# Kernel tuning notes

Hardware: AMD Instinct MI355X
Metric: run time of the kernel (lower is better)

Reference implementation:

```python
import jax, jax.numpy as jnp
import numpy as np

B, L, D, NHEADS, P = 64, 256, 768, 8, 3
VOCAB, DEP, NLAYERS = 30522, 45, 2
LAM = 0.5


def _forward(src_mask, aspect_mask, lex, attention_mask,
             tok_emb, seg_emb, pool_w, pool_b, ln_a, ln_b,
             dep_emb, fc1_w, fc1_b, fc2_w, fc2_b,
             aq_w, aq_b, ak_w, ak_b, lq_w, lq_b, lk_w, lk_b, root_w,
             gcn_w, gcn_b, fc3_w, fc3_b, cls_w, cls_b, vlin_w,
             text_bert_indices, bert_segments_ids, ori_tag, head):
    b, l = text_bert_indices.shape
    d = tok_emb.shape[1]
    dk = d // NHEADS
    NEG = jnp.float32(-1e30)
    # stand-in BERT encoder: token + segment embeddings, tanh pooler on [CLS]
    seq = tok_emb[text_bert_indices] + seg_emb[bert_segments_ids]
    pooled = jnp.tanh(seq[:, 0] @ pool_w + pool_b)
    # torch LayerNorm variant: unbiased std (ddof=1)
    mean = seq.mean(-1, keepdims=True)
    std = jnp.std(seq, axis=-1, keepdims=True, ddof=1)
    gcn_in = ln_a * (seq - mean) / (std + 1e-6) + ln_b
    # in-place fmask[:,0]=1 mutates src_mask storage in torch -> effective mask
    sm = src_mask.at[:, 0].set(1.0)
    # dependency-tag score -> per-token softmax -> scatter into [L,L] adjacency
    dep_h = jax.nn.relu(dep_emb[ori_tag] @ fc1_w + fc1_b)
    dep_s = (dep_h @ fc2_w + fc2_b)[..., 0]                      # [B,L]
    dep_feat = jax.nn.softmax(dep_s * sm + (1.0 - sm) * NEG, axis=1)
    to_idx = jnp.arange(1, l)
    fro = head[:, :l - 1]                                        # [B,L-1]
    b_idx = jnp.arange(b)[:, None]
    vals = dep_feat[:, :l - 1]
    dep_adj = jnp.ones((b, l, l), jnp.float32)
    dep_adj = dep_adj.at[b_idx, fro, to_idx[None, :]].set(vals)
    dep_adj = dep_adj.at[b_idx, to_idx[None, :], fro].set(vals)
    # multi-head attention-as-adjacency (returns softmax weights only)
    q = (gcn_in @ aq_w + aq_b).reshape(b, l, NHEADS, dk).transpose(0, 2, 1, 3)
    k = (gcn_in @ ak_w + ak_b).reshape(b, l, NHEADS, dk).transpose(0, 2, 1, 3)
    scores = jnp.einsum('bhqd,bhkd->bhqk', q, k) / (jnp.sqrt(jnp.float32(dk)) + 1e-9)
    scores = jnp.where(sm[:, None, None, :] == 0, jnp.float32(-1e9), scores)
    adj_ag = jax.nn.softmax(scores, axis=-1).mean(axis=1)        # [B,L,L]
    eye = jnp.eye(l, dtype=jnp.float32)
    adj_ag = (adj_ag * (1.0 - eye) + eye) * sm[:, :, None]
    # structured latent attention (stand-in for missing StructuredAtt):
    # masked bilinear attention biased by dep_adj + root attention loss
    q2 = gcn_in @ lq_w + lq_b
    k2 = gcn_in @ lk_w + lk_b
    lat = jnp.einsum('bqd,bkd->bqk', q2, k2) / jnp.sqrt(jnp.float32(d))
    lat = lat + dep_adj + (1.0 - sm)[:, None, :] * (-10000.0)
    adj_latent = jax.nn.softmax(lat, axis=-1)
    root_p = jax.nn.softmax((gcn_in @ root_w)[..., 0] * sm + (1.0 - sm) * NEG, axis=1)
    loss_root = -jnp.mean(jnp.log(jnp.sum(root_p * aspect_mask, axis=1) + 1e-9))
    adj_latent = (adj_latent * (1.0 - eye) + eye) * sm[:, :, None]
    # gated dual-adjacency GCN layers
    H_l = gcn_in
    I_sem = gcn_in
    for layer in range(gcn_w.shape[0]):
        g_l = jax.nn.sigmoid(H_l)
        I_sem = (adj_ag @ H_l) @ gcn_w[layer] + gcn_b[layer]
        I_lat = (adj_latent @ H_l) @ gcn_w[layer] + gcn_b[layer]
        g = jax.nn.sigmoid(I_lat)
        lam_g = LAM * g
        I_com = (1.0 - lam_g) * I_sem + lam_g * I_lat
        H_out = jax.nn.relu(I_com @ fc3_w + fc3_b)
        H_l = g_l * H_out + (1.0 - g_l) * H_l
    # readout
    asp_wn = aspect_mask.sum(axis=1, keepdims=True)              # [B,1]
    m3 = sm[:, :, None]
    h_l = H_l * m3
    h_sem = I_sem * m3
    beta = jnp.einsum('bqd,bkd->bqk', h_l, h_sem) / 1000.0
    attn_o = jax.nn.softmax(beta.sum(axis=1, keepdims=True), axis=2)  # [B,1,L]
    outputs = (attn_o @ I_sem)[:, 0]                             # [B,D]
    sem_pool = (I_sem * aspect_mask[:, :, None]).sum(axis=1) / (asp_wn + 1e-9)
    final = jnp.concatenate([outputs, sem_pool, pooled], axis=-1)  # [B,3D]
    logits = final @ cls_w + cls_b
    e = (H_l @ vlin_w)[..., 0]
    lw = jax.nn.softmax(e, axis=1) * 50.0
    lw = lw * sm.at[:, 0].set(0.0)
    lexicon_loss = jnp.mean((lw - lex) ** 2)
    return logits, loss_root, lexicon_loss


def setup_inputs() -> dict:
    key = jax.random.key(0)
    ks = jax.random.split(key, 24)
    s = 0.02
    n = lambda i, shape: jax.random.normal(ks[i], shape, dtype=jnp.float32) * s
    inp = {}
    inp['text_bert_indices'] = jax.random.randint(ks[0], (B, L), 0, VOCAB, dtype=jnp.int32)
    inp['bert_segments_ids'] = jnp.zeros((B, L), jnp.int32)
    inp['attention_mask'] = jnp.ones((B, L), jnp.float32)
    inp['src_mask'] = jnp.ones((B, L), jnp.float32)
    inp['aspect_mask'] = jax.random.randint(ks[1], (B, L), 0, 2).astype(jnp.float32)
    inp['lex'] = jax.random.uniform(ks[2], (B, L), dtype=jnp.float32)
    inp['ori_tag'] = jax.random.randint(ks[3], (B, L), 0, DEP, dtype=jnp.int32)
    inp['head'] = jax.random.randint(ks[4], (B, L), 0, L, dtype=jnp.int32)
    inp['tok_emb'] = n(5, (VOCAB, D)); inp['seg_emb'] = n(6, (2, D))
    inp['pool_w'] = n(7, (D, D)); inp['pool_b'] = jnp.zeros((D,), jnp.float32)
    inp['ln_a'] = jnp.ones((D,), jnp.float32); inp['ln_b'] = jnp.zeros((D,), jnp.float32)
    inp['dep_emb'] = n(8, (DEP, 300))
    inp['fc1_w'] = n(9, (300, 256)); inp['fc1_b'] = jnp.zeros((256,), jnp.float32)
    inp['fc2_w'] = n(10, (256, 1)); inp['fc2_b'] = jnp.zeros((1,), jnp.float32)
    inp['aq_w'] = n(11, (D, D)); inp['aq_b'] = jnp.zeros((D,), jnp.float32)
    inp['ak_w'] = n(12, (D, D)); inp['ak_b'] = jnp.zeros((D,), jnp.float32)
    inp['lq_w'] = n(13, (D, D)); inp['lq_b'] = jnp.zeros((D,), jnp.float32)
    inp['lk_w'] = n(14, (D, D)); inp['lk_b'] = jnp.zeros((D,), jnp.float32)
    inp['root_w'] = n(15, (D, 1))
    inp['gcn_w'] = n(16, (NLAYERS, D, D)); inp['gcn_b'] = jnp.zeros((NLAYERS, D), jnp.float32)
    inp['fc3_w'] = n(17, (D, D)); inp['fc3_b'] = jnp.zeros((D,), jnp.float32)
    inp['cls_w'] = n(18, (3 * D, P)); inp['cls_b'] = jnp.zeros((P,), jnp.float32)
    inp['vlin_w'] = n(19, (D, 1))
    return inp


def reference(text_bert_indices, bert_segments_ids, attention_mask, src_mask, aspect_mask, lex,
              ori_tag, head, tok_emb, seg_emb, pool_w, pool_b, ln_a, ln_b, dep_emb,
              fc1_w, fc1_b, fc2_w, fc2_b, aq_w, aq_b, ak_w, ak_b, lq_w, lq_b, lk_w, lk_b,
              root_w, gcn_w, gcn_b, fc3_w, fc3_b, cls_w, cls_b, vlin_w):
    return _forward(src_mask, aspect_mask, lex, attention_mask,
                    tok_emb, seg_emb, pool_w, pool_b, ln_a, ln_b,
                    dep_emb, fc1_w, fc1_b, fc2_w, fc2_b,
                    aq_w, aq_b, ak_w, ak_b, lq_w, lq_b, lk_w, lk_b, root_w,
                    gcn_w, gcn_b, fc3_w, fc3_b, cls_w, cls_b, vlin_w,
                    text_bert_indices, bert_segments_ids, ori_tag, head)
```

## Files before the change

### kernel.cpp

```cpp
#include <hip/hip_runtime.h>
#include <hip/hip_bf16.h>
#include <math.h>

#define DI __device__ __forceinline__

constexpr int cB = 64, cL = 256, cD = 768;
constexpr long BLD = (long)cB * cL * cD;
constexpr long BLL = (long)cB * cL * cL;
constexpr long cLL = (long)cL * cL;
constexpr long cLD = (long)cL * cD;

typedef __attribute__((ext_vector_type(8))) short b8;
typedef __attribute__((ext_vector_type(4))) float f4;

#define GLDS(g, l)                                                    \
  __builtin_amdgcn_global_load_lds(                                   \
      (const __attribute__((address_space(1))) void*)(g),             \
      (__attribute__((address_space(3))) void*)(l), 16, 0, 0)

#define SCB __builtin_amdgcn_sched_barrier(0)
DI void rbar() { SCB; __builtin_amdgcn_s_barrier(); SCB; }
DI void lbar() {
  asm volatile("s_waitcnt lgkmcnt(0)" ::: "memory");
  SCB;
  __builtin_amdgcn_s_barrier();
  SCB;
}

DI float wsum(float v) {
#pragma unroll
  for (int o = 32; o > 0; o >>= 1) v += __shfl_down(v, o, 64);
  return v;
}
DI float wsum_all(float v) {
#pragma unroll
  for (int m = 32; m > 0; m >>= 1) v += __shfl_xor(v, m, 64);
  return v;
}
DI float wmaxr(float v) {
#pragma unroll
  for (int o = 32; o > 0; o >>= 1) v = fmaxf(v, __shfl_down(v, o, 64));
  return v;
}
DI float blockSum(float v) {
  __shared__ float sh[4];
  v = wsum(v);
  __syncthreads();
  if ((threadIdx.x & 63) == 0) sh[threadIdx.x >> 6] = v;
  __syncthreads();
  return sh[0] + sh[1] + sh[2] + sh[3];
}
DI float blockMax(float v) {
  __shared__ float sh[4];
  v = wmaxr(v);
  __syncthreads();
  if ((threadIdx.x & 63) == 0) sh[threadIdx.x >> 6] = v;
  __syncthreads();
  return fmaxf(fmaxf(sh[0], sh[1]), fmaxf(sh[2], sh[3]));
}
DI float sigf(float x) { return 1.f / (1.f + expf(-x)); }

template <int OBF, int RELU, int BIAS, int EPI, int SWZ>
__global__ __launch_bounds__(256, 2) void bgemm(
    const __hip_bfloat16* __restrict__ A, const __hip_bfloat16* __restrict__ BT,
    void* __restrict__ Cv, const float* __restrict__ bias,
    float* __restrict__ auxf, __hip_bfloat16* __restrict__ auxb,
    int K, int lda, int ldb, int ldc,
    int zshift, int zmask, long sA1, long sA2, long sB1, long sB2, long sC,
    int czdiv) {
  __shared__ __hip_bfloat16 Asp[128 * 32];
  __shared__ __hip_bfloat16 Bsp[128 * 32];
  int bx = blockIdx.x, by = blockIdx.y;
  if (SWZ) {
    int gx = gridDim.x;
    int nb = gx * gridDim.y;
    int id = by * gx + bx;
    int cpx = nb >> 3;
    id = (id & 7) * cpx + (id >> 3);
    bx = id % gx;
    by = id / gx;
  }
  int z = blockIdx.z;
  A += (long)(z >> zshift) * sA1 + (long)(z & zmask) * sA2;
  BT += (long)(z >> zshift) * sB1 + (long)(z & zmask) * sB2;
  int tid = threadIdx.x;
  int lane = tid & 63, w = tid >> 6;
  int wr = w >> 1, wc = w & 1;
  int l16 = lane & 15, q = lane >> 4;
  int m0 = by << 7, n0 = bx << 7;

  int fm = tid >> 2, fq = tid & 3;
  const __hip_bfloat16* Ap0 = A + (long)(m0 + fm) * lda + fq * 8;
  const __hip_bfloat16* Ap1 = A + (long)(m0 + fm + 64) * lda + fq * 8;
  const __hip_bfloat16* Bp0 = BT + (long)(n0 + fm) * ldb + fq * 8;
  const __hip_bfloat16* Bp1 = BT + (long)(n0 + fm + 64) * ldb + fq * 8;
  char* Aw0 = (char*)Asp + (w << 10);
  char* Aw1 = (char*)Asp + 4096 + (w << 10);
  char* Bw0 = (char*)Bsp + (w << 10);
  char* Bw1 = (char*)Bsp + 4096 + (w << 10);

  f4 acc[4][4];
#pragma unroll
  for (int i = 0; i < 4; i++)
#pragma unroll
    for (int j = 0; j < 4; j++) acc[i][j] = (f4){0.f, 0.f, 0.f, 0.f};

  for (int k0 = 0; k0 < K; k0 += 32) {
    GLDS(Ap0 + k0, Aw0);
    GLDS(Ap1 + k0, Aw1);
    GLDS(Bp0 + k0, Bw0);
    GLDS(Bp1 + k0, Bw1);
    __syncthreads();
    b8 af[4], bf[4];
#pragma unroll
    for (int i = 0; i < 4; i++)
      af[i] = *(const b8*)&Asp[(wr * 64 + i * 16 + l16) * 32 + q * 8];
#pragma unroll
    for (int j = 0; j < 4; j++)
      bf[j] = *(const b8*)&Bsp[(wc * 64 + j * 16 + l16) * 32 + q * 8];
#pragma unroll
    for (int i = 0; i < 4; i++)
#pragma unroll
      for (int j = 0; j < 4; j++)
        acc[i][j] = __builtin_amdgcn_mfma_f32_16x16x32_bf16(af[i], bf[j], acc[i][j], 0, 0, 0);
    __syncthreads();
  }
  if (EPI == 4) {
#pragma unroll
    for (int j = 0; j < 4; j++) {
      int n = n0 + wc * 64 + j * 16 + l16;
#pragma unroll
      for (int i = 0; i < 4; i++) {
        int m = m0 + wr * 64 + i * 16 + (q << 2);
        __hip_bfloat16 t4[4];
#pragma unroll
        for (int r = 0; r < 4; r++) t4[r] = __float2bfloat16(acc[i][j][r]);
        long bidx = (long)(m >> 8) * sC + (long)n * cL + (m & 255);
        *(uint2*)&((__hip_bfloat16*)Cv)[bidx] = *(uint2*)t4;
      }
    }
    return;
  }
  long cz = (long)(z >> czdiv) * sC;
#pragma unroll
  for (int j = 0; j < 4; j++) {
    int n = n0 + wc * 64 + j * 16 + l16;
    float bv = BIAS ? bias[n] : 0.f;
#pragma unroll
    for (int i = 0; i < 4; i++) {
#pragma unroll
      for (int r = 0; r < 4; r++) {
        int m = m0 + wr * 64 + i * 16 + q * 4 + r;
        long idx = cz + (long)m * ldc + n;
        float v = acc[i][j][r] + bv;
        if (EPI == 0) {
          if (RELU) v = fmaxf(v, 0.f);
          if (OBF)
            ((__hip_bfloat16*)Cv)[idx] = __float2bfloat16(v);
          else
            ((float*)Cv)[idx] = v;
        } else {
          v = fmaxf(v, 0.f);
          float h = __bfloat162float(auxb[idx]);
          float g = sigf(h);
          float o = h + g * (v - h);
          auxb[idx] = __float2bfloat16(o);
          if (auxf) auxf[idx] = o;
        }
      }
    }
  }
}

__global__ __launch_bounds__(256, 2) void bgemm_dual(
    const __hip_bfloat16* __restrict__ A1g, const __hip_bfloat16* __restrict__ A2g,
    const __hip_bfloat16* __restrict__ BTg, float* __restrict__ IsemF,
    __hip_bfloat16* __restrict__ Icb, const float* __restrict__ bias,
    int write_isem) {
  __shared__ __hip_bfloat16 A1sp[128 * 32];
  __shared__ __hip_bfloat16 A2sp[128 * 32];
  __shared__ __hip_bfloat16 Bsp[128 * 32];
  int id = (blockIdx.z * 2 + blockIdx.y) * 6 + blockIdx.x;
  id = (id & 7) * 96 + (id >> 3);
  int bx = id % 6, t = id / 6;
  int by = t & 1, z = t >> 1;
  const __hip_bfloat16* A1 = A1g + (long)z * cLL;
  const __hip_bfloat16* A2 = A2g + (long)z * cLL;
  const __hip_bfloat16* BT = BTg + (long)z * cLD;
  int tid = threadIdx.x;
  int lane = tid & 63, w = tid >> 6;
  int wr = w >> 1, wc = w & 1;
  int l16 = lane & 15, q = lane >> 4;
  int m0 = by << 7, n0 = bx << 7;

  int fm = tid >> 2, fq = tid & 3;
  const __hip_bfloat16* A1p0 = A1 + (long)(m0 + fm) * cL + fq * 8;
  const __hip_bfloat16* A1p1 = A1p0 + 64L * cL;
  const __hip_bfloat16* A2p0 = A2 + (long)(m0 + fm) * cL + fq * 8;
  const __hip_bfloat16* A2p1 = A2p0 + 64L * cL;
  const __hip_bfloat16* Bp0 = BT + (long)(n0 + fm) * cL + fq * 8;
  const __hip_bfloat16* Bp1 = Bp0 + 64L * cL;
  char* w10 = (char*)A1sp + (w << 10);
  char* w11 = (char*)A1sp + 4096 + (w << 10);
  char* w20 = (char*)A2sp + (w << 10);
  char* w21 = (char*)A2sp + 4096 + (w << 10);
  char* wb0 = (char*)Bsp + (w << 10);
  char* wb1 = (char*)Bsp + 4096 + (w << 10);

  f4 ac1[4][4], ac2[4][4];
#pragma unroll
  for (int i = 0; i < 4; i++)
#pragma unroll
    for (int j = 0; j < 4; j++) {
      ac1[i][j] = (f4){0.f, 0.f, 0.f, 0.f};
      ac2[i][j] = (f4){0.f, 0.f, 0.f, 0.f};
    }

  for (int k0 = 0; k0 < cL; k0 += 32) {
    GLDS(A1p0 + k0, w10);
    GLDS(A1p1 + k0, w11);
    GLDS(A2p0 + k0, w20);
    GLDS(A2p1 + k0, w21);
    GLDS(Bp0 + k0, wb0);
    GLDS(Bp1 + k0, wb1);
    __syncthreads();
    b8 a1f[4], a2f[4], bf[4];
#pragma unroll
    for (int i = 0; i < 4; i++) {
      a1f[i] = *(const b8*)&A1sp[(wr * 64 + i * 16 + l16) * 32 + q * 8];
      a2f[i] = *(const b8*)&A2sp[(wr * 64 + i * 16 + l16) * 32 + q * 8];
    }
#pragma unroll
    for (int j = 0; j < 4; j++)
      bf[j] = *(const b8*)&Bsp[(wc * 64 + j * 16 + l16) * 32 + q * 8];
#pragma unroll
    for (int i = 0; i < 4; i++)
#pragma unroll
      for (int j = 0; j < 4; j++) {
        ac1[i][j] = __builtin_amdgcn_mfma_f32_16x16x32_bf16(a1f[i], bf[j], ac1[i][j], 0, 0, 0);
        ac2[i][j] = __builtin_amdgcn_mfma_f32_16x16x32_bf16(a2f[i], bf[j], ac2[i][j], 0, 0, 0);
      }
    __syncthreads();
  }
  long cz = (long)z * cLD;
#pragma unroll
  for (int j = 0; j < 4; j++) {
    int n = n0 + wc * 64 + j * 16 + l16;
    float bv = bias[n];
#pragma unroll
    for (int i = 0; i < 4; i++) {
#pragma unroll
      for (int r = 0; r < 4; r++) {
        int m = m0 + wr * 64 + i * 16 + q * 4 + r;
        long idx = cz + (long)m * cD + n;
        float is = ac1[i][j][r] + bv;
        float il = ac2[i][j][r] + bv;
        float g = 0.5f * sigf(il);
        Icb[idx] = __float2bfloat16(is + g * (il - is));
        if (write_isem) IsemF[idx] = is;
      }
    }
  }
}

__global__ __launch_bounds__(256, 2) void k_qkadj2(
    const __hip_bfloat16* __restrict__ qkb, const float* __restrict__ src_mask,
    const int* __restrict__ headv, const float* __restrict__ df,
    __hip_bfloat16* __restrict__ outAag, __hip_bfloat16* __restrict__ outAlat) {
  __shared__ __hip_bfloat16 Qs[2][64 * 32];
  __shared__ __hip_bfloat16 Ks[2][256 * 32];
  __shared__ float red[4][64];
  int id = (blockIdx.z * gridDim.y + blockIdx.y) * gridDim.x + blockIdx.x;
  int W = (id & 7) * 64 + (id >> 3);
  const bool lat = W >= 256;
  int rem = W & 255;
  const int b = rem >> 2, m0 = (rem & 3) << 6;
  const int QOFF = lat ? 1536 : 0;
  const int KOFF = lat ? 2304 : 768;
  const float scale = lat ? (1.f / sqrtf(768.f)) : (1.f / (sqrtf(96.f) + 1e-9f));
  const int tid = threadIdx.x, lane = tid & 63, w = tid >> 6;
  const int l16 = lane & 15, q = lane >> 4;
  const long rowbase = (long)b * cL;
  const __hip_bfloat16* Qg =
      qkb + (rowbase + m0 + (tid >> 2)) * 3072 + (tid & 3) * 8 + QOFF;
  const __hip_bfloat16* Kg =
      qkb + (rowbase + (tid >> 2)) * 3072 + (tid & 3) * 8 + KOFF;

  float smj[4];
#pragma unroll
  for (int j = 0; j < 4; j++) {
    int col = w * 64 + j * 16 + l16;
    smj[j] = (col == 0) ? 1.f : src_mask[b * cL + col];
  }

  f4 sa[4][4], aag[4][4];
#pragma unroll
  for (int i = 0; i < 4; i++)
#pragma unroll
    for (int j = 0; j < 4; j++) {
      sa[i][j] = (f4){0.f, 0.f, 0.f, 0.f};
      aag[i][j] = (f4){0.f, 0.f, 0.f, 0.f};
    }

  auto STAGE = [&](int s, int p) {
    GLDS(Qg + s * 32, (char*)Qs[p] + (w << 10));
#pragma unroll
    for (int u = 0; u < 4; u++)
      GLDS(Kg + (long)u * 196608 + s * 32, (char*)Ks[p] + u * 4096 + (w << 10));
  };

  STAGE(0, 0);
  STAGE(1, 1);

  for (int s = 0; s < 24; s++) {
    const int p = s & 1;
    if (s < 23) {
      asm volatile("s_waitcnt vmcnt(5)" ::: "memory");
    } else {
      asm volatile("s_waitcnt vmcnt(0)" ::: "memory");
    }
    rbar();
    if (!lat && (s % 3) == 0) {
#pragma unroll
      for (int i = 0; i < 4; i++)
#pragma unroll
        for (int j = 0; j < 4; j++) sa[i][j] = (f4){0.f, 0.f, 0.f, 0.f};
    }
    b8 af[4], bf[4];
#pragma unroll
    for (int i = 0; i < 4; i++)
      af[i] = *(const b8*)&Qs[p][(i * 16 + l16) * 32 + q * 8];
#pragma unroll
    for (int j = 0; j < 4; j++)
      bf[j] = *(const b8*)&Ks[p][(w * 64 + j * 16 + l16) * 32 + q * 8];
#pragma unroll
    for (int i = 0; i < 4; i++)
#pragma unroll
      for (int j = 0; j < 4; j++)
        sa[i][j] = __builtin_amdgcn_mfma_f32_16x16x32_bf16(af[i], bf[j], sa[i][j], 0, 0, 0);
    rbar();
    if (s + 2 < 24) STAGE(s + 2, p);
    if (!lat && (s % 3) == 2) {
#pragma unroll
      for (int i = 0; i < 4; i++)
#pragma unroll
        for (int j = 0; j < 4; j++)
#pragma unroll
          for (int r = 0; r < 4; r++)
            sa[i][j][r] = (smj[j] == 0.f) ? -1e9f : sa[i][j][r] * scale;
      float rm_[4][4];
#pragma unroll
      for (int i = 0; i < 4; i++)
#pragma unroll
        for (int r = 0; r < 4; r++) {
          float m = fmaxf(fmaxf(sa[i][0][r], sa[i][1][r]), fmaxf(sa[i][2][r], sa[i][3][r]));
#pragma unroll
          for (int o = 1; o < 16; o <<= 1) m = fmaxf(m, __shfl_xor(m, o, 64));
          if (l16 == 0) red[w][i * 16 + q * 4 + r] = m;
        }
      lbar();
#pragma unroll
      for (int i = 0; i < 4; i++)
#pragma unroll
        for (int r = 0; r < 4; r++) {
          int lr = i * 16 + q * 4 + r;
          rm_[i][r] = fmaxf(fmaxf(red[0][lr], red[1][lr]), fmaxf(red[2][lr], red[3][lr]));
        }
      lbar();
#pragma unroll
      for (int i = 0; i < 4; i++)
#pragma unroll
        for (int r = 0; r < 4; r++) {
          float s0 = 0.f;
#pragma unroll
          for (int j = 0; j < 4; j++) {
            float e = expf(sa[i][j][r] - rm_[i][r]);
            sa[i][j][r] = e;
            s0 += e;
          }
#pragma unroll
          for (int o = 1; o < 16; o <<= 1) s0 += __shfl_xor(s0, o, 64);
          if (l16 == 0) red[w][i * 16 + q * 4 + r] = s0;
        }
      lbar();
#pragma unroll
      for (int i = 0; i < 4; i++)
#pragma unroll
        for (int r = 0; r < 4; r++) {
          int lr = i * 16 + q * 4 + r;
          float iv = 1.f / (red[0][lr] + red[1][lr] + red[2][lr] + red[3][lr]);
#pragma unroll
          for (int j = 0; j < 4; j++) aag[i][j][r] += sa[i][j][r] * iv;
        }
    }
  }

  float inv_[4][4];
  if (lat) {
    int hcol[4];
    float dfc[4];
#pragma unroll
    for (int j = 0; j < 4; j++) {
      int col = w * 64 + j * 16 + l16;
      hcol[j] = (col >= 1) ? headv[b * cL + col - 1] : -1;
      dfc[j] = (col >= 1) ? df[b * cL + col - 1] : 0.f;
    }
    int hrow_[4][4];
    float dfr_[4][4];
#pragma unroll
    for (int i = 0; i < 4; i++)
#pragma unroll
      for (int r = 0; r < 4; r++) {
        int grow = m0 + i * 16 + q * 4 + r;
        hrow_[i][r] = (grow >= 1) ? headv[b * cL + grow - 1] : -1;
        dfr_[i][r] = (grow >= 1) ? df[b * cL + grow - 1] : 0.f;
      }
#pragma unroll
    for (int i = 0; i < 4; i++)
#pragma unroll
      for (int j = 0; j < 4; j++) {
        int col = w * 64 + j * 16 + l16;
#pragma unroll
        for (int r = 0; r < 4; r++) {
          int grow = m0 + i * 16 + q * 4 + r;
          float dep = 1.f;
          if (hcol[j] == grow) dep = dfc[j];
          if (col == hrow_[i][r]) dep = dfr_[i][r];
          sa[i][j][r] = sa[i][j][r] * scale + dep + (1.f - smj[j]) * -10000.f;
        }
      }
    float rm_[4][4];
#pragma unroll
    for (int i = 0; i < 4; i++)
#pragma unroll
      for (int r = 0; r < 4; r++) {
        float m = fmaxf(fmaxf(sa[i][0][r], sa[i][1][r]), fmaxf(sa[i][2][r], sa[i][3][r]));
#pragma unroll
        for (int o = 1; o < 16; o <<= 1) m = fmaxf(m, __shfl_xor(m, o, 64));
        if (l16 == 0) red[w][i * 16 + q * 4 + r] = m;
      }
    lbar();
#pragma unroll
    for (int i = 0; i < 4; i++)
#pragma unroll
      for (int r = 0; r < 4; r++) {
        int lr = i * 16 + q * 4 + r;
        rm_[i][r] = fmaxf(fmaxf(red[0][lr], red[1][lr]), fmaxf(red[2][lr], red[3][lr]));
      }
    lbar();
#pragma unroll
    for (int i = 0; i < 4; i++)
#pragma unroll
      for (int r = 0; r < 4; r++) {
        float s0 = 0.f;
#pragma unroll
        for (int j = 0; j < 4; j++) {
          float e = expf(sa[i][j][r] - rm_[i][r]);
          sa[i][j][r] = e;
          s0 += e;
        }
#pragma unroll
        for (int o = 1; o < 16; o <<= 1) s0 += __shfl_xor(s0, o, 64);
        if (l16 == 0) red[w][i * 16 + q * 4 + r] = s0;
      }
    lbar();
#pragma unroll
    for (int i = 0; i < 4; i++)
#pragma unroll
      for (int r = 0; r < 4; r++) {
        int lr = i * 16 + q * 4 + r;
        inv_[i][r] = 1.f / (red[0][lr] + red[1][lr] + red[2][lr] + red[3][lr]);
      }
  }

  float smi_[4][4];
#pragma unroll
  for (int i = 0; i < 4; i++)
#pragma unroll
    for (int r = 0; r < 4; r++) {
      int grow = m0 + i * 16 + q * 4 + r;
      smi_[i][r] = (grow == 0) ? 1.f : src_mask[b * cL + grow];
    }
  __hip_bfloat16* outA = lat ? outAlat : outAag;
#pragma unroll
  for (int j = 0; j < 4; j++) {
    int col = w * 64 + j * 16 + l16;
#pragma unroll
    for (int i = 0; i < 4; i++)
#pragma unroll
      for (int r = 0; r < 4; r++) {
        int grow = m0 + i * 16 + q * 4 + r;
        float p = lat ? sa[i][j][r] * inv_[i][r] : aag[i][j][r] * 0.125f;
        float v = (col == grow) ? 1.f : p;
        outA[((long)b * cL + grow) * cL + col] = __float2bfloat16(v * smi_[i][r]);
      }
  }
}

__global__ void k_wconv7(const float* __restrict__ s0, const float* __restrict__ s1,
                         const float* __restrict__ s2, const float* __restrict__ s3,
                         const float* __restrict__ s4, const float* __restrict__ s5,
                         const float* __restrict__ s6, __hip_bfloat16* __restrict__ dst,
                         const float* __restrict__ ba, const float* __restrict__ bb,
                         const float* __restrict__ bc, const float* __restrict__ bd,
                         float* __restrict__ catb) {
  if (blockIdx.z == 7) {
    if (blockIdx.y != 0 || blockIdx.x >= 12) return;
    int tid = threadIdx.y * 32 + threadIdx.x;
    int i = blockIdx.x * 256 + tid;
    float v = (i < 768) ? ba[i] : (i < 1536) ? bb[i - 768]
              : (i < 2304) ? bc[i - 1536] : bd[i - 2304];
    catb[i] = v;
    return;
  }
  const float* srcs[7] = {s0, s1, s2, s3, s4, s5, s6};
  const float* src = srcs[blockIdx.z];
  __hip_bfloat16* d = dst + (long)blockIdx.z * cD * cD;
  __shared__ float t[32][33];
  int k0 = blockIdx.x * 32, n0 = blockIdx.y * 32;
  int tx = threadIdx.x, ty = threadIdx.y;
#pragma unroll
  for (int i = 0; i < 32; i += 8) t[ty + i][tx] = src[(long)(k0 + ty + i) * cD + n0 + tx];
  __syncthreads();
#pragma unroll
  for (int i = 0; i < 32; i += 8)
    d[(long)(n0 + ty + i) * cD + k0 + tx] = __float2bfloat16(t[tx][ty + i]);
}

__global__ __launch_bounds__(256) void k_gcnin(
    const int* __restrict__ tbi, const int* __restrict__ bsi,
    const float* __restrict__ tok, const float* __restrict__ seg,
    const float* __restrict__ ln_a, const float* __restrict__ ln_b,
    const float* __restrict__ root_w, __hip_bfloat16* __restrict__ gib,
    float* __restrict__ x64, float* __restrict__ e1) {
  int wave = threadIdx.x >> 6, lane = threadIdx.x & 63;
  long bl = (long)blockIdx.x * 4 + wave;
  int t = tbi[bl], s = bsi[bl];
  const float* tr = tok + (long)t * cD;
  const float* sr = seg + (long)s * cD;
  float x[12];
  float ls = 0.f;
#pragma unroll
  for (int c = 0; c < 12; c++) {
    int d = lane + (c << 6);
    x[c] = tr[d] + sr[d];
    ls += x[c];
  }
  if ((bl & 255) == 0) {
#pragma unroll
    for (int c = 0; c < 12; c++) x64[(bl >> 8) * cD + lane + (c << 6)] = x[c];
  }
  float mean = wsum_all(ls) * (1.f / 768.f);
  float lv = 0.f;
#pragma unroll
  for (int c = 0; c < 12; c++) { float d2 = x[c] - mean; lv += d2 * d2; }
  float var = wsum_all(lv) * (1.f / 767.f);
  float inv = 1.f / (sqrtf(var) + 1e-6f);
  float rdot = 0.f;
#pragma unroll
  for (int c = 0; c < 12; c++) {
    int d = lane + (c << 6);
    float v = ln_a[d] * (x[c] - mean) * inv + ln_b[d];
    gib[bl * cD + d] = __float2bfloat16(v);
    rdot += v * root_w[d];
  }
  float tot = wsum_all(rdot);
  if (lane == 0) e1[bl] = tot;
}

__global__ __launch_bounds__(256) void k_pool1(
    const float* __restrict__ x64, const float* __restrict__ pw,
    float* __restrict__ pacc) {
  __shared__ float pws[48][256];
  __shared__ float xs[16][48];
  int i0 = blockIdx.x * 48, j0 = blockIdx.y * 256, b0 = blockIdx.z * 16;
  for (int r = 0; r < 48; r++) pws[r][threadIdx.x] = pw[(long)(i0 + r) * cD + j0 + threadIdx.x];
  for (int idx = threadIdx.x; idx < 16 * 48; idx += 256)
    xs[idx / 48][idx % 48] = x64[(long)(b0 + idx / 48) * cD + i0 + idx % 48];
  __syncthreads();
  int j = threadIdx.x;
  for (int b = 0; b < 16; b++) {
    float acc = 0.f;
#pragma unroll 8
    for (int i = 0; i < 48; i++) acc += xs[b][i] * pws[i][j];
    atomicAdd(&pacc[(long)(b0 + b) * cD + j0 + j], acc);
  }
}

__global__ __launch_bounds__(256) void k_s45(
    const float* __restrict__ dep_emb, const float* __restrict__ fc1w,
    const float* __restrict__ fc1b, const float* __restrict__ fc2w,
    const float* __restrict__ fc2b, float* __restrict__ s45) {
  int t = blockIdx.x;
  __shared__ float e[300];
  for (int i = threadIdx.x; i < 300; i += 256) e[i] = dep_emb[t * 300 + i];
  __syncthreads();
  int j = threadIdx.x;
  float h = fc1b[j];
  for (int i = 0; i < 300; i++) h += e[i] * fc1w[i * 256 + j];
  h = fmaxf(h, 0.f);
  float tot = blockSum(h * fc2w[j]);
  if (threadIdx.x == 0) s45[t] = tot + fc2b[0];
}

__global__ __launch_bounds__(256) void k_depfeat(
    const int* __restrict__ ori, const float* __restrict__ src_mask,
    const float* __restrict__ s45, float* __restrict__ dep_feat) {
  int b = blockIdx.x, l = threadIdx.x;
  float smv = (l == 0) ? 1.f : src_mask[b * cL + l];
  float sc = s45[ori[b * cL + l]] * smv + (1.f - smv) * (-1e30f);
  float mx = blockMax(sc);
  float ex = expf(sc - mx);
  float sum = blockSum(ex);
  dep_feat[b * cL + l] = ex / sum;
}

__global__ __launch_bounds__(256) void k_rowdot2(
    const float* __restrict__ Isem, const float* __restrict__ hlsum,
    const float* __restrict__ gcnH, const float* __restrict__ vlin,
    float* __restrict__ sraw, float* __restrict__ e2) {
  int r = blockIdx.x * 4 + (threadIdx.x >> 6);
  int lane = threadIdx.x & 63;
  bool z = blockIdx.y != 0;
  const float4* row = (const float4*)((z ? gcnH : Isem) + (long)r * cD);
  const float4* wp = z ? (const float4*)vlin
                       : (const float4*)(hlsum + (long)(r >> 8) * cD);
  float s = 0.f;
#pragma unroll
  for (int c = 0; c < 3; c++) {
    int idx = c * 64 + lane;
    float4 a = row[idx], b = wp[idx];
    s += a.x * b.x + a.y * b.y + a.z * b.z + a.w * b.w;
  }
  s = wsum(s);
  if (lane == 0) (z ? e2 : sraw)[r] = s;
}

__global__ __launch_bounds__(256) void k_tailred(
    const float* __restrict__ sraw, const float* __restrict__ e1,
    const float* __restrict__ e2, const float* __restrict__ src_mask,
    const float* __restrict__ aspect_mask, const float* __restrict__ lex,
    float* __restrict__ wgt, float* __restrict__ asum,
    float* __restrict__ out_root, float* __restrict__ out_lex) {
  int b = blockIdx.x, l = threadIdx.x;
  float smv = (l == 0) ? 1.f : src_mask[b * cL + l];
  float am = aspect_mask[b * cL + l];
  float s = sraw[b * cL + l] * smv * 0.001f;
  float mx = blockMax(s);
  float ex = expf(s - mx);
  float sum = blockSum(ex);
  wgt[b * cL + l] = ex / sum;
  float a = blockSum(am);
  if (l == 0) asum[b] = a;
  float sc = e1[b * cL + l] * smv + (1.f - smv) * (-1e30f);
  float mx2 = blockMax(sc);
  float ex2 = expf(sc - mx2);
  float sum2 = blockSum(ex2);
  float tot = blockSum((ex2 / sum2) * am);
  if (l == 0) atomicAdd(out_root, -logf(tot + 1e-9f) * (1.f / 64.f));
  float e = e2[b * cL + l];
  float mx3 = blockMax(e);
  float ex3 = expf(e - mx3);
  float sum3 = blockSum(ex3);
  float mult = (l == 0) ? 0.f : src_mask[b * cL + l];
  float lw = ex3 / sum3 * 50.f * mult;
  float d2 = lw - lex[b * cL + l];
  float t3 = blockSum(d2 * d2);
  if (l == 0) atomicAdd(out_lex, t3 * (1.f / (64.f * 256.f)));
}

__global__ __launch_bounds__(256) void k_hl(
    const float* __restrict__ H, const float* __restrict__ src_mask,
    float* __restrict__ hlsum) {
  int b = blockIdx.z, d = (blockIdx.y << 8) + threadIdx.x, l0 = blockIdx.x * 32;
  float acc = 0.f;
  for (int l = l0; l < l0 + 32; l++) {
    float smv = (l == 0) ? 1.f : src_mask[b * cL + l];
    acc += H[((long)b * cL + l) * cD + d] * smv;
  }
  atomicAdd(&hlsum[(long)b * cD + d], acc);
}

__global__ __launch_bounds__(256) void k_wsum(
    const float* __restrict__ Isem, const float* __restrict__ wgt,
    const float* __restrict__ am, float* __restrict__ outputs,
    float* __restrict__ sempool) {
  int b = blockIdx.z, d = (blockIdx.y << 8) + threadIdx.x, l0 = blockIdx.x * 32;
  float accO = 0.f, accS = 0.f;
  for (int l = l0; l < l0 + 32; l++) {
    float v = Isem[((long)b * cL + l) * cD + d];
    accO += wgt[b * cL + l] * v;
    accS += am[b * cL + l] * v;
  }
  atomicAdd(&outputs[(long)b * cD + d], accO);
  atomicAdd(&sempool[(long)b * cD + d], accS);
}

__global__ __launch_bounds__(256) void k_logits(
    const float* __restrict__ outputs, const float* __restrict__ sempool,
    const float* __restrict__ pacc, const float* __restrict__ pb,
    const float* __restrict__ asum, const float* __restrict__ cw,
    const float* __restrict__ cb, float* __restrict__ out) {
  int b = blockIdx.x;
  float inv = 1.f / (asum[b] + 1e-9f);
  float a0 = 0.f, a1 = 0.f, a2 = 0.f;
  for (int i = threadIdx.x; i < 3 * cD; i += 256) {
    float f;
    if (i < cD)
      f = outputs[(long)b * cD + i];
    else if (i < 2 * cD)
      f = sempool[(long)b * cD + i - cD] * inv;
    else
      f = tanhf(pacc[(long)b * cD + i - 2 * cD] + pb[i - 2 * cD]);
    a0 += f * cw[i * 3 + 0];
    a1 += f * cw[i * 3 + 1];
    a2 += f * cw[i * 3 + 2];
  }
  a0 = blockSum(a0);
  a1 = blockSum(a1);
  a2 = blockSum(a2);
  if (threadIdx.x == 0) {
    out[b * 3 + 0] = a0 + cb[0];
    out[b * 3 + 1] = a1 + cb[1];
    out[b * 3 + 2] = a2 + cb[2];
  }
}

extern "C" void kernel_launch(void* const* d_in, const int* in_sizes, int n_in,
                              void* d_out, int out_size, void* d_ws, size_t ws_size,
                              hipStream_t stream) {
  const int* tbi = (const int*)d_in[0];
  const int* bsi = (const int*)d_in[1];
  const float* src_mask = (const float*)d_in[3];
  const float* aspect_mask = (const float*)d_in[4];
  const float* lex = (const float*)d_in[5];
  const int* ori = (const int*)d_in[6];
  const int* head = (const int*)d_in[7];
  const float* tok_emb = (const float*)d_in[8];
  const float* seg_emb = (const float*)d_in[9];
  const float* pool_w = (const float*)d_in[10];
  const float* pool_b = (const float*)d_in[11];
  const float* ln_a = (const float*)d_in[12];
  const float* ln_b = (const float*)d_in[13];
  const float* dep_emb = (const float*)d_in[14];
  const float* fc1_w = (const float*)d_in[15];
  const float* fc1_b = (const float*)d_in[16];
  const float* fc2_w = (const float*)d_in[17];
  const float* fc2_b = (const float*)d_in[18];
  const float* aq_w = (const float*)d_in[19];
  const float* aq_b = (const float*)d_in[20];
  const float* ak_w = (const float*)d_in[21];
  const float* ak_b = (const float*)d_in[22];
  const float* lq_w = (const float*)d_in[23];
  const float* lq_b = (const float*)d_in[24];
  const float* lk_w = (const float*)d_in[25];
  const float* lk_b = (const float*)d_in[26];
  const float* root_w = (const float*)d_in[27];
  const float* gcn_w = (const float*)d_in[28];
  const float* gcn_b = (const float*)d_in[29];
  const float* fc3_w = (const float*)d_in[30];
  const float* fc3_b = (const float*)d_in[31];
  const float* cls_w = (const float*)d_in[32];
  const float* cls_b = (const float*)d_in[33];
  const float* vlin_w = (const float*)d_in[34];

  float* out = (float*)d_out;
  float* ws = (float*)d_ws;
  float* gcnH = ws;
  float* Isem = gcnH + BLD;
  float* depfeat = Isem + BLD;
  float* s45 = depfeat + cB * cL;
  float* pooled = s45 + 64;
  float* x64 = pooled + cB * cD;
  float* hlsum = x64 + cB * cD;
  float* outputs = hlsum + cB * cD;
  float* sempool = outputs + cB * cD;
  float* pacc = sempool + cB * cD;
  float* e1 = pacc + cB * cD;
  float* e2 = e1 + cB * cL;
  float* sraw = e2 + cB * cL;
  float* wgt = sraw + cB * cL;
  float* asum = wgt + cB * cL;
  float* catb = asum + 64;
  __hip_bfloat16* gib = (__hip_bfloat16*)(catb + 3072);
  __hip_bfloat16* qkb = gib + BLD;
  __hip_bfloat16* scores = qkb + 4 * BLD;
  __hip_bfloat16* adjag_b = scores + 8 * BLL;
  __hip_bfloat16* adjlat_b = adjag_b + BLL;
  __hip_bfloat16* wbt = adjlat_b + BLL;
  __hip_bfloat16* HWbT = qkb + BLD;
  __hip_bfloat16* Icb = qkb + 2 * BLD;

  hipMemsetAsync((char*)d_out + 192 * sizeof(float), 0, 2 * sizeof(float), stream);
  hipMemsetAsync(hlsum, 0, 4 * cB * cD * sizeof(float), stream);

  k_gcnin<<<cB * cL / 4, 256, 0, stream>>>(tbi, bsi, tok_emb, seg_emb, ln_a, ln_b,
                                           root_w, gib, x64, e1);
  k_s45<<<45, 256, 0, stream>>>(dep_emb, fc1_w, fc1_b, fc2_w, fc2_b, s45);
  k_depfeat<<<cB, 256, 0, stream>>>(ori, src_mask, s45, depfeat);
  k_pool1<<<dim3(16, 3, 4), 256, 0, stream>>>(x64, pool_w, pacc);
  k_wconv7<<<dim3(24, 24, 8), dim3(32, 8), 0, stream>>>(
      aq_w, ak_w, lq_w, lk_w, gcn_w, gcn_w + (long)cD * cD, fc3_w, wbt,
      aq_b, ak_b, lq_b, lk_b, catb);

  const long DD = (long)cD * cD;
  const long LD = cLD;

  bgemm<1, 0, 1, 0, 1><<<dim3(24, 128, 1), 256, 0, stream>>>(
      gib, wbt, qkb, catb, nullptr, nullptr, cD, cD, cD, 3072,
      0, 0, 0, 0, 0, 0, 0, 0);

  k_qkadj2<<<dim3(4, cB, 2), 256, 0, stream>>>(qkb, src_mask, head, depfeat,
                                               adjag_b, adjlat_b);

  for (int layer = 0; layer < 2; layer++) {
    const float* bb = gcn_b + (long)layer * cD;
    bgemm<1, 0, 0, 4, 1><<<dim3(6, 128, 1), 256, 0, stream>>>(
        gib, wbt + (4 + layer) * DD, HWbT, nullptr, nullptr, nullptr,
        cD, cD, cD, cD, 0, 0, 0, 0, 0, 0, LD, 0);
    bgemm_dual<<<dim3(6, 2, cB), 256, 0, stream>>>(
        adjag_b, adjlat_b, HWbT, Isem, Icb, bb, layer == 1 ? 1 : 0);
    bgemm<0, 1, 1, 2, 1><<<dim3(6, 128, 1), 256, 0, stream>>>(
        Icb, wbt + 6 * DD, nullptr, fc3_b, layer == 1 ? gcnH : nullptr, gib,
        cD, cD, cD, cD, 0, 0, 0, 0, 0, 0, 0, 0);
  }

  k_hl<<<dim3(8, 3, cB), 256, 0, stream>>>(gcnH, src_mask, hlsum);
  k_rowdot2<<<dim3(cB * cL / 4, 2), 256, 0, stream>>>(Isem, hlsum, gcnH, vlin_w,
                                                      sraw, e2);
  k_tailred<<<cB, 256, 0, stream>>>(sraw, e1, e2, src_mask, aspect_mask, lex,
                                    wgt, asum, out + 192, out + 193);
  k_wsum<<<dim3(8, 3, cB), 256, 0, stream>>>(Isem, wgt, aspect_mask, outputs, sempool);
  k_logits<<<cB, 256, 0, stream>>>(outputs, sempool, pacc, pool_b, asum,
                                   cls_w, cls_b, out);
}
```

Measured before the change: 727.6 us.

## Double-buffer GEMM LDS loads and fuse layer-0 GCN weight GEMM into QK projection

```diff
diff --git a/kernel.cpp b/kernel.cpp
--- a/kernel.cpp
+++ b/kernel.cpp
@@ -68,8 +68,8 @@
     int K, int lda, int ldb, int ldc,
     int zshift, int zmask, long sA1, long sA2, long sB1, long sB2, long sC,
     int czdiv) {
-  __shared__ __hip_bfloat16 Asp[128 * 32];
-  __shared__ __hip_bfloat16 Bsp[128 * 32];
+  __shared__ __hip_bfloat16 Asp[2][128 * 32];
+  __shared__ __hip_bfloat16 Bsp[2][128 * 32];
   int bx = blockIdx.x, by = blockIdx.y;
   if (SWZ) {
     int gx = gridDim.x;
@@ -105,25 +105,38 @@
 #pragma unroll
     for (int j = 0; j < 4; j++) acc[i][j] = (f4){0.f, 0.f, 0.f, 0.f};
 
-  for (int k0 = 0; k0 < K; k0 += 32) {
-    GLDS(Ap0 + k0, Aw0);
-    GLDS(Ap1 + k0, Aw1);
-    GLDS(Bp0 + k0, Bw0);
-    GLDS(Bp1 + k0, Bw1);
-    __syncthreads();
+  const int nk = K >> 5;
+  auto STG = [&](int s, int p) {
+    int k0 = s << 5;
+    int bo = p << 13;
+    GLDS(Ap0 + k0, Aw0 + bo);
+    GLDS(Ap1 + k0, Aw1 + bo);
+    GLDS(Bp0 + k0, Bw0 + bo);
+    GLDS(Bp1 + k0, Bw1 + bo);
+  };
+  STG(0, 0);
+  STG(1, 1);
+  for (int s = 0; s < nk; s++) {
+    const int p = s & 1;
+    if (s < nk - 1)
+      asm volatile("s_waitcnt vmcnt(4)" ::: "memory");
+    else
+      asm volatile("s_waitcnt vmcnt(0)" ::: "memory");
+    rbar();
     b8 af[4], bf[4];
 #pragma unroll
     for (int i = 0; i < 4; i++)
-      af[i] = *(const b8*)&Asp[(wr * 64 + i * 16 + l16) * 32 + q * 8];
+      af[i] = *(const b8*)&Asp[p][(wr * 64 + i * 16 + l16) * 32 + q * 8];
 #pragma unroll
     for (int j = 0; j < 4; j++)
-      bf[j] = *(const b8*)&Bsp[(wc * 64 + j * 16 + l16) * 32 + q * 8];
+      bf[j] = *(const b8*)&Bsp[p][(wc * 64 + j * 16 + l16) * 32 + q * 8];
 #pragma unroll
     for (int i = 0; i < 4; i++)
 #pragma unroll
       for (int j = 0; j < 4; j++)
         acc[i][j] = __builtin_amdgcn_mfma_f32_16x16x32_bf16(af[i], bf[j], acc[i][j], 0, 0, 0);
-    __syncthreads();
+    rbar();
+    if (s + 2 < nk) STG(s + 2, p);
   }
   if (EPI == 4) {
 #pragma unroll
@@ -141,31 +154,44 @@
     }
     return;
   }
-  long cz = (long)(z >> czdiv) * sC;
+  long cz = (long)(z >> czdiv) * ((EPI == 5) ? 0 : sC);
 #pragma unroll
   for (int j = 0; j < 4; j++) {
     int n = n0 + wc * 64 + j * 16 + l16;
-    float bv = BIAS ? bias[n] : 0.f;
-#pragma unroll
-    for (int i = 0; i < 4; i++) {
-#pragma unroll
-      for (int r = 0; r < 4; r++) {
-        int m = m0 + wr * 64 + i * 16 + q * 4 + r;
-        long idx = cz + (long)m * ldc + n;
-        float v = acc[i][j][r] + bv;
-        if (EPI == 0) {
-          if (RELU) v = fmaxf(v, 0.f);
-          if (OBF)
-            ((__hip_bfloat16*)Cv)[idx] = __float2bfloat16(v);
-          else
-            ((float*)Cv)[idx] = v;
-        } else {
-          v = fmaxf(v, 0.f);
-          float h = __bfloat162float(auxb[idx]);
-          float g = sigf(h);
-          float o = h + g * (v - h);
-          auxb[idx] = __float2bfloat16(o);
-          if (auxf) auxf[idx] = o;
+    if (EPI == 5 && n >= 3072) {
+      int np = n - 3072;
+#pragma unroll
+      for (int i = 0; i < 4; i++) {
+        int m = m0 + wr * 64 + i * 16 + (q << 2);
+        __hip_bfloat16 t4[4];
+#pragma unroll
+        for (int r = 0; r < 4; r++) t4[r] = __float2bfloat16(acc[i][j][r]);
+        long bidx = (long)(m >> 8) * sC + (long)np * cL + (m & 255);
+        *(uint2*)&auxb[bidx] = *(uint2*)t4;
+      }
+    } else {
+      float bv = BIAS ? bias[n] : 0.f;
+#pragma unroll
+      for (int i = 0; i < 4; i++) {
+#pragma unroll
+        for (int r = 0; r < 4; r++) {
+          int m = m0 + wr * 64 + i * 16 + q * 4 + r;
+          long idx = cz + (long)m * ldc + n;
+          float v = acc[i][j][r] + bv;
+          if (EPI == 0 || EPI == 5) {
+            if (RELU) v = fmaxf(v, 0.f);
+            if (OBF)
+              ((__hip_bfloat16*)Cv)[idx] = __float2bfloat16(v);
+            else
+              ((float*)Cv)[idx] = v;
+          } else {
+            v = fmaxf(v, 0.f);
+            float h = __bfloat162float(auxb[idx]);
+            float g = sigf(h);
+            float o = h + g * (v - h);
+            auxb[idx] = __float2bfloat16(o);
+            if (auxf) auxf[idx] = o;
+          }
         }
       }
     }
@@ -177,9 +203,9 @@
     const __hip_bfloat16* __restrict__ BTg, float* __restrict__ IsemF,
     __hip_bfloat16* __restrict__ Icb, const float* __restrict__ bias,
     int write_isem) {
-  __shared__ __hip_bfloat16 A1sp[128 * 32];
-  __shared__ __hip_bfloat16 A2sp[128 * 32];
-  __shared__ __hip_bfloat16 Bsp[128 * 32];
+  __shared__ __hip_bfloat16 A1sp[2][128 * 32];
+  __shared__ __hip_bfloat16 A2sp[2][128 * 32];
+  __shared__ __hip_bfloat16 Bsp[2][128 * 32];
   int id = (blockIdx.z * 2 + blockIdx.y) * 6 + blockIdx.x;
   id = (id & 7) * 96 + (id >> 3);
   int bx = id % 6, t = id / 6;
@@ -216,23 +242,34 @@
       ac2[i][j] = (f4){0.f, 0.f, 0.f, 0.f};
     }
 
-  for (int k0 = 0; k0 < cL; k0 += 32) {
-    GLDS(A1p0 + k0, w10);
-    GLDS(A1p1 + k0, w11);
-    GLDS(A2p0 + k0, w20);
-    GLDS(A2p1 + k0, w21);
-    GLDS(Bp0 + k0, wb0);
-    GLDS(Bp1 + k0, wb1);
-    __syncthreads();
+  auto STG = [&](int s, int p) {
+    int k0 = s << 5;
+    int bo = p << 13;
+    GLDS(A1p0 + k0, w10 + bo);
+    GLDS(A1p1 + k0, w11 + bo);
+    GLDS(A2p0 + k0, w20 + bo);
+    GLDS(A2p1 + k0, w21 + bo);
+    GLDS(Bp0 + k0, wb0 + bo);
+    GLDS(Bp1 + k0, wb1 + bo);
+  };
+  STG(0, 0);
+  STG(1, 1);
+  for (int s = 0; s < 8; s++) {
+    const int p = s & 1;
+    if (s < 7)
+      asm volatile("s_waitcnt vmcnt(6)" ::: "memory");
+    else
+      asm volatile("s_waitcnt vmcnt(0)" ::: "memory");
+    rbar();
     b8 a1f[4], a2f[4], bf[4];
 #pragma unroll
     for (int i = 0; i < 4; i++) {
-      a1f[i] = *(const b8*)&A1sp[(wr * 64 + i * 16 + l16) * 32 + q * 8];
-      a2f[i] = *(const b8*)&A2sp[(wr * 64 + i * 16 + l16) * 32 + q * 8];
+      a1f[i] = *(const b8*)&A1sp[p][(wr * 64 + i * 16 + l16) * 32 + q * 8];
+      a2f[i] = *(const b8*)&A2sp[p][(wr * 64 + i * 16 + l16) * 32 + q * 8];
     }
 #pragma unroll
     for (int j = 0; j < 4; j++)
-      bf[j] = *(const b8*)&Bsp[(wc * 64 + j * 16 + l16) * 32 + q * 8];
+      bf[j] = *(const b8*)&Bsp[p][(wc * 64 + j * 16 + l16) * 32 + q * 8];
 #pragma unroll
     for (int i = 0; i < 4; i++)
 #pragma unroll
@@ -240,7 +277,8 @@
         ac1[i][j] = __builtin_amdgcn_mfma_f32_16x16x32_bf16(a1f[i], bf[j], ac1[i][j], 0, 0, 0);
         ac2[i][j] = __builtin_amdgcn_mfma_f32_16x16x32_bf16(a2f[i], bf[j], ac2[i][j], 0, 0, 0);
       }
-    __syncthreads();
+    rbar();
+    if (s + 2 < 8) STG(s + 2, p);
   }
   long cz = (long)z * cLD;
 #pragma unroll
@@ -788,7 +826,7 @@
   __hip_bfloat16* adjag_b = scores + 8 * BLL;
   __hip_bfloat16* adjlat_b = adjag_b + BLL;
   __hip_bfloat16* wbt = adjlat_b + BLL;
-  __hip_bfloat16* HWbT = qkb + BLD;
+  __hip_bfloat16* HWbT = scores;
   __hip_bfloat16* Icb = qkb + 2 * BLD;
 
   hipMemsetAsync((char*)d_out + 192 * sizeof(float), 0, 2 * sizeof(float), stream);
@@ -806,24 +844,28 @@
   const long DD = (long)cD * cD;
   const long LD = cLD;
 
-  bgemm<1, 0, 1, 0, 1><<<dim3(24, 128, 1), 256, 0, stream>>>(
-      gib, wbt, qkb, catb, nullptr, nullptr, cD, cD, cD, 3072,
-      0, 0, 0, 0, 0, 0, 0, 0);
+  bgemm<1, 0, 1, 5, 1><<<dim3(30, 128, 1), 256, 0, stream>>>(
+      gib, wbt, qkb, catb, nullptr, HWbT, cD, cD, cD, 3072,
+      0, 0, 0, 0, 0, 0, LD, 0);
 
   k_qkadj2<<<dim3(4, cB, 2), 256, 0, stream>>>(qkb, src_mask, head, depfeat,
                                                adjag_b, adjlat_b);
 
-  for (int layer = 0; layer < 2; layer++) {
-    const float* bb = gcn_b + (long)layer * cD;
-    bgemm<1, 0, 0, 4, 1><<<dim3(6, 128, 1), 256, 0, stream>>>(
-        gib, wbt + (4 + layer) * DD, HWbT, nullptr, nullptr, nullptr,
-        cD, cD, cD, cD, 0, 0, 0, 0, 0, 0, LD, 0);
-    bgemm_dual<<<dim3(6, 2, cB), 256, 0, stream>>>(
-        adjag_b, adjlat_b, HWbT, Isem, Icb, bb, layer == 1 ? 1 : 0);
-    bgemm<0, 1, 1, 2, 1><<<dim3(6, 128, 1), 256, 0, stream>>>(
-        Icb, wbt + 6 * DD, nullptr, fc3_b, layer == 1 ? gcnH : nullptr, gib,
-        cD, cD, cD, cD, 0, 0, 0, 0, 0, 0, 0, 0);
-  }
+  bgemm_dual<<<dim3(6, 2, cB), 256, 0, stream>>>(
+      adjag_b, adjlat_b, HWbT, Isem, Icb, gcn_b, 0);
+  bgemm<0, 1, 1, 2, 1><<<dim3(6, 128, 1), 256, 0, stream>>>(
+      Icb, wbt + 6 * DD, nullptr, fc3_b, nullptr, gib,
+      cD, cD, cD, cD, 0, 0, 0, 0, 0, 0, 0, 0);
+
+  bgemm<1, 0, 0, 4, 1><<<dim3(6, 128, 1), 256, 0, stream>>>(
+      gib, wbt + 5 * DD, HWbT, nullptr, nullptr, nullptr,
+      cD, cD, cD, cD, 0, 0, 0, 0, 0, 0, LD, 0);
+
+  bgemm_dual<<<dim3(6, 2, cB), 256, 0, stream>>>(
+      adjag_b, adjlat_b, HWbT, Isem, Icb, gcn_b + cD, 1);
+  bgemm<0, 1, 1, 2, 1><<<dim3(6, 128, 1), 256, 0, stream>>>(
+      Icb, wbt + 6 * DD, nullptr, fc3_b, gcnH, gib,
+      cD, cD, cD, cD, 0, 0, 0, 0, 0, 0, 0, 0);
 
   k_hl<<<dim3(8, 3, cB), 256, 0, stream>>>(gcnH, src_mask, hlsum);
   k_rowdot2<<<dim3(cB * cL / 4, 2), 256, 0, stream>>>(Isem, hlsum, gcnH, vlin_w,
```

New measurement: 729.6 us. About the same (+0.3%).
